# Performance work log

Measured on AMD Instinct MI355X. Metric: run time of the kernel, lower is better.

## Reference

```python
import jax, jax.numpy as jnp
import numpy as np

K = 3          # kernel_size
PAD = K // 2   # unfold padding
BN_EPS = 1e-5


def _conv(x, w, dilation, pad):
    # x: [B,C,H,W], w: [O,I,kh,kw]
    return jax.lax.conv_general_dilated(
        x, w, window_strides=(1, 1), padding=[(pad, pad), (pad, pad)],
        rhs_dilation=(dilation, dilation),
        dimension_numbers=("NCHW", "OIHW", "NCHW"))


def _bn(x, g, b, rm, rv):
    # eval-mode batchnorm with running stats
    inv = g / jnp.sqrt(rv + BN_EPS)
    return x * inv[None, :, None, None] + (b - rm * inv)[None, :, None, None]


def setup_inputs() -> dict:
    key = jax.random.key(0)
    ks = jax.random.split(key, 8)
    B, T, H, W = 8, 5, 512, 512
    mid = 16  # max(16, T // 4)
    inp = {
        "x_aligned": jax.random.normal(ks[0], (B, T, H, W), jnp.float32),
        "raw_diff": jax.random.normal(ks[1], (B, T - 1, H, W), jnp.float32),
        "w1": jax.random.normal(ks[2], (mid, T, 3, 3), jnp.float32) * 0.1,
        "g1": jnp.ones((mid,), jnp.float32), "b1": jnp.zeros((mid,), jnp.float32),
        "rm1": jnp.zeros((mid,), jnp.float32), "rv1": jnp.ones((mid,), jnp.float32),
        "w2": jax.random.normal(ks[3], (mid, mid, 3, 3), jnp.float32) * 0.1,
        "g2": jnp.ones((mid,), jnp.float32), "b2": jnp.zeros((mid,), jnp.float32),
        "rm2": jnp.zeros((mid,), jnp.float32), "rv2": jnp.ones((mid,), jnp.float32),
        "w3": jax.random.normal(ks[4], (mid, mid, 3, 3), jnp.float32) * 0.1,
        "g3": jnp.ones((mid,), jnp.float32), "b3": jnp.zeros((mid,), jnp.float32),
        "rm3": jnp.zeros((mid,), jnp.float32), "rv3": jnp.ones((mid,), jnp.float32),
        "w4": jax.random.normal(ks[5], (T * K * K, mid, 1, 1), jnp.float32) * 0.1,
        "bias": jnp.full((1,), -1.0, jnp.float32),
    }
    return inp


def reference(x_aligned, raw_diff, w1, g1, b1, rm1, rv1, w2, g2, b2, rm2, rv2,
              w3, g3, b3, rm3, rv3, w4, bias):
    B, T, H, W = x_aligned.shape
    # _accumulate: sequential abs-add == sum of abs over frame-diff axis
    acc = jnp.sum(jnp.abs(raw_diff), axis=1, keepdims=True)  # [B,1,H,W]
    mean = jnp.mean(acc)
    n = acc.size
    std = jnp.sqrt(jnp.sum((acc - mean) ** 2) / (n - 1))  # unbiased (torch default)
    motion = (acc - mean) / (std + 1e-6)
    motion_seq = jnp.broadcast_to(motion, (B, T, H, W))
    # _generate_kernel: conv+BN+ReLU stack with dilations 1,2,4 then 1x1
    h = jax.nn.relu(_bn(_conv(motion_seq, w1, 1, 1), g1, b1, rm1, rv1))
    h = jax.nn.relu(_bn(_conv(h, w2, 2, 2), g2, b2, rm2, rv2))
    h = jax.nn.relu(_bn(_conv(h, w3, 4, 4), g3, b3, rm3, rv3))
    raw_kernel = _conv(h, w4, 1, 0).reshape(B, T, K * K, H, W)
    kernel = (jax.nn.sigmoid(raw_kernel + bias[0]) + 0.01) * 10.0
    # _enhance: unfold (KxK patches, zero pad) then per-pixel weighted sum
    xp = jnp.pad(x_aligned, ((0, 0), (0, 0), (PAD, PAD), (PAD, PAD)))
    patches = jnp.stack(
        [xp[:, :, i:i + H, j:j + W] for i in range(K) for j in range(K)],
        axis=2)  # [B,T,K*K,H,W], matches F.unfold row-major kernel order
    return jnp.sum(kernel * patches, axis=2)  # [B,T,H,W]
```

## Files before the change

kernel.cpp:

```cpp
#include <hip/hip_runtime.h>
#include <hip/hip_bf16.h>
#include <math.h>

#define HH 512
#define WW 512
#define BB 8
#define TT 5
#define MID 16
#define HWSZ (HH*WW)
#define NPIX (BB*HWSZ)

typedef __attribute__((ext_vector_type(8))) short bf16x8;
typedef __attribute__((ext_vector_type(4))) float f32x4;

__device__ inline unsigned short f2bf(float f){
  unsigned u = __float_as_uint(f);
  u = u + 0x7fffu + ((u >> 16) & 1u);
  return (unsigned short)(u >> 16);
}
__device__ inline unsigned packpair(float a, float b){
  unsigned ua = __float_as_uint(a) + 0x8000u;
  unsigned ub = __float_as_uint(b) + 0x8000u;
  return __builtin_amdgcn_perm(ub, ua, 0x07060302u);
}
__device__ inline float blo(unsigned u){ return __uint_as_float(u << 16); }
__device__ inline float bhi(unsigned u){ return __uint_as_float(u & 0xffff0000u); }

union U4B { uint4 u; bf16x8 h; };


__global__ __launch_bounds__(256) void k_acc(const float* __restrict__ rd,
                                             float4* __restrict__ acc,
                                             float2* __restrict__ partial){
  int t = blockIdx.x * 256 + threadIdx.x;
  int i = t << 2;
  int b = i >> 18, p = i & (HWSZ - 1);
  const float* base = rd + (size_t)b * 4 * HWSZ + p;
  float4 f0 = *(const float4*)(base);
  float4 f1 = *(const float4*)(base + HWSZ);
  float4 f2 = *(const float4*)(base + 2*HWSZ);
  float4 f3 = *(const float4*)(base + 3*HWSZ);
  float4 s4;
  s4.x = fabsf(f0.x) + fabsf(f1.x) + fabsf(f2.x) + fabsf(f3.x);
  s4.y = fabsf(f0.y) + fabsf(f1.y) + fabsf(f2.y) + fabsf(f3.y);
  s4.z = fabsf(f0.z) + fabsf(f1.z) + fabsf(f2.z) + fabsf(f3.z);
  s4.w = fabsf(f0.w) + fabsf(f1.w) + fabsf(f2.w) + fabsf(f3.w);
  acc[t] = s4;
  float s  = s4.x + s4.y + s4.z + s4.w;
  float s2 = s4.x*s4.x + s4.y*s4.y + s4.z*s4.z + s4.w*s4.w;
  #pragma unroll
  for (int off = 32; off; off >>= 1){
    s  += __shfl_down(s,  off);
    s2 += __shfl_down(s2, off);
  }
  __shared__ float ls[4], ls2[4];
  int lane = threadIdx.x & 63, wid = threadIdx.x >> 6;
  if (lane == 0){ ls[wid] = s; ls2[wid] = s2; }
  __syncthreads();
  if (threadIdx.x == 0)
    partial[blockIdx.x] = make_float2(ls[0]+ls[1]+ls[2]+ls[3],
                                      ls2[0]+ls2[1]+ls2[2]+ls2[3]);
}

__global__ __launch_bounds__(256) void k_prep(const float2* __restrict__ partial,
    const float* __restrict__ w1, const float* __restrict__ w2, const float* __restrict__ w3,
    const float* __restrict__ g1, const float* __restrict__ b1, const float* __restrict__ rm1, const float* __restrict__ rv1,
    const float* __restrict__ g2, const float* __restrict__ b2, const float* __restrict__ rm2, const float* __restrict__ rv2,
    const float* __restrict__ g3, const float* __restrict__ b3, const float* __restrict__ rm3, const float* __restrict__ rv3,
    const float* __restrict__ w4, const float* __restrict__ bias0,
    float* __restrict__ cst, unsigned* __restrict__ wsB2, unsigned* __restrict__ wsB3,
    uint4* __restrict__ wsB4){
  int t = threadIdx.x;
  double s = 0.0, s2 = 0.0;
  for (int j = t; j < 2048; j += 256){
    float2 v = partial[j];
    s += (double)v.x; s2 += (double)v.y;
  }
  #pragma unroll
  for (int off = 32; off; off >>= 1){
    s  += __shfl_down(s,  off);
    s2 += __shfl_down(s2, off);
  }
  __shared__ double ds[4], ds2[4];
  int lane = t & 63, wid = t >> 6;
  if (lane == 0){ ds[wid] = s; ds2[wid] = s2; }
  __syncthreads();
  if (t == 0){
    double S  = ds[0]+ds[1]+ds[2]+ds[3];
    double S2 = ds2[0]+ds2[1]+ds2[2]+ds2[3];
    double n = (double)NPIX;
    double mean = S / n;
    double var  = (S2 - n * mean * mean) / (n - 1.0);
    double sd   = sqrt(var);
    cst[0] = (float)mean;
    cst[1] = (float)(1.0 / (sd + 1e-6));
    cst[242] = bias0[0];
  }
  if (t < 144){
    int c = t / 9, k = t % 9;
    float sw = 0.f;
    for (int f = 0; f < TT; f++) sw += w1[c*45 + f*9 + k];
    cst[2 + t] = sw;
  }
  if (t < 16){
    float s1 = g1[t] * rsqrtf(rv1[t] + 1e-5f);
    cst[146 + t] = s1; cst[162 + t] = b1[t] - rm1[t] * s1;
    float c2 = g2[t] * rsqrtf(rv2[t] + 1e-5f);
    cst[288 + t] = c2; cst[304 + t] = b2[t] - rm2[t] * c2;
    float c3 = g3[t] * rsqrtf(rv3[t] + 1e-5f);
    cst[320 + t] = c3; cst[336 + t] = b3[t] - rm3[t] * c3;
  }
  for (int it = 0; it < 5; it++){
    int idx = it * 256 + t;
    int m = idx >> 8, rem = idx & 255;
    int L = rem >> 2, jj = rem & 3;
    int out = L & 15, q = L >> 4;
    unsigned v2 = 0, v3 = 0;
    #pragma unroll
    for (int h = 0; h < 2; h++){
      int j = 2*jj + h;
      int k = q*8 + j;
      int tap = 2*m + (k >> 4);
      int ci = k & 15;
      unsigned bv2 = 0, bv3 = 0;
      if (tap < 9){
        bv2 = f2bf(w2[out*144 + ci*9 + tap]);
        bv3 = f2bf(w3[out*144 + ci*9 + tap]);
      }
      v2 |= bv2 << (16*h);
      v3 |= bv3 << (16*h);
    }
    wsB2[idx] = v2; wsB3[idx] = v3;
  }
  if (t < 192){
    int c = t >> 6, L = t & 63;
    int n = L & 15, q = L >> 4;
    int o = c*16 + n;
    unsigned vv[4];
    #pragma unroll
    for (int jj = 0; jj < 4; jj++){
      unsigned pk = 0;
      #pragma unroll
      for (int h = 0; h < 2; h++){
        int j = 2*jj + h, kci = q*8 + j;
        unsigned bv = 0;
        if (kci < 16 && o < 45) bv = f2bf(w4[o*16 + kci]);
        pk |= bv << (16*h);
      }
      vv[jj] = pk;
    }
    wsB4[c*64 + L] = make_uint4(vv[0], vv[1], vv[2], vv[3]);
  }
}

#define TR 12
#define TC 68
__global__ __launch_bounds__(256) void k_conv12(const float* __restrict__ acc,
                                                const float* __restrict__ C,
                                                const unsigned* __restrict__ wsB2,
                                                uint2* __restrict__ h2){
  __shared__ uint4 PL[2][TR*TC];
  int tid = threadIdx.x;
  int blk = blockIdx.x;
  int xt = blk & 7, yt = (blk >> 3) & 63, b = blk >> 9;
  int y0 = yt << 3, x0 = xt << 6;
  float mean = C[0], inv = C[1];
  const float* ab = acc + ((size_t)b << 18);
  #pragma unroll
  for (int it = 0; it < 4; it++){
    int i = it*256 + tid;
    if (i < TR*TC){
      int r = (i * 241) >> 14;
      int p = i - r*TC;
      int gy = y0 - 2 + r, gx = x0 - 2 + p;
      uint4 lo = make_uint4(0u,0u,0u,0u), hi = lo;
      if ((unsigned)gy < HH && (unsigned)gx < WW){
        float a[MID];
        #pragma unroll
        for (int o = 0; o < MID; o++) a[o] = 0.f;
        #pragma unroll
        for (int ky = 0; ky < 3; ky++){
          int yy = gy + ky - 1;
          if ((unsigned)yy >= HH) continue;
          #pragma unroll
          for (int kx = 0; kx < 3; kx++){
            int xx = gx + kx - 1;
            if ((unsigned)xx >= WW) continue;
            float m = (ab[(yy << 9) + xx] - mean) * inv;
            int k = ky * 3 + kx;
            #pragma unroll
            for (int o = 0; o < MID; o++) a[o] = fmaf(C[2 + o*9 + k], m, a[o]);
          }
        }
        unsigned pk[8];
        #pragma unroll
        for (int j = 0; j < 8; j++){
          float v0 = fmaxf(0.f, fmaf(a[2*j],   C[146 + 2*j],   C[162 + 2*j]));
          float v1 = fmaxf(0.f, fmaf(a[2*j+1], C[146 + 2*j+1], C[162 + 2*j+1]));
          pk[j] = packpair(v0, v1);
        }
        lo = make_uint4(pk[0], pk[1], pk[2], pk[3]);
        hi = make_uint4(pk[4], pk[5], pk[6], pk[7]);
      }
      PL[0][r*TC + p] = lo;
      PL[1][r*TC + p] = hi;
    }
  }
  __syncthreads();
  int lane = tid & 63, wv = tid >> 6;
  int col = lane & 15, q = lane >> 4;
  int chSel = q & 1;
  bool hiTap = (q >= 2);
  uint4 wfrag[5];
  #pragma unroll
  for (int m = 0; m < 5; m++) wfrag[m] = ((const uint4*)wsB2)[m*64 + lane];
  float4 sc = *(const float4*)&C[288 + q*4];
  float4 bi = *(const float4*)&C[304 + q*4];
  #pragma unroll
  for (int rr = 0; rr < 2; rr++){
    int ly = wv*2 + rr;
    #pragma unroll
    for (int g = 0; g < 4; g++){
      int lx = g << 4;
      f32x4 cc = {0.f, 0.f, 0.f, 0.f};
      #pragma unroll
      for (int m = 0; m < 5; m++){
        const int ta = 2*m, tb = 2*m + 1;
        int dy = (hiTap ? tb/3 : ta/3) - 1;
        int dx = (hiTap ? tb%3 : ta%3) - 1;
        bool tv = hiTap ? (tb < 9) : true;
        int trow = ly + 2 + 2*dy;
        int tpx  = lx + 2 + col + 2*dx;
        U4B bv; bv.u = PL[chSel][trow*TC + tpx];
        if (!tv) bv.u = make_uint4(0u,0u,0u,0u);
        U4B wb; wb.u = wfrag[m];
        cc = __builtin_amdgcn_mfma_f32_16x16x32_bf16(wb.h, bv.h, cc, 0, 0, 0);
      }
      float v0 = fmaxf(0.f, fmaf(cc[0], sc.x, bi.x));
      float v1 = fmaxf(0.f, fmaf(cc[1], sc.y, bi.y));
      float v2 = fmaxf(0.f, fmaf(cc[2], sc.z, bi.z));
      float v3 = fmaxf(0.f, fmaf(cc[3], sc.w, bi.w));
      int gy = y0 + ly, gx = x0 + lx + col;
      h2[(size_t)((b << 18) | (gy << 9) | gx)*4 + q] =
          make_uint2(packpair(v0, v1), packpair(v2, v3));
    }
  }
}

template<int DIL>
__device__ inline f32x4 convW(const uint4* __restrict__ hin, const uint4 wfrag[5],
                              int b, int y, int x0, int col, int q, f32x4 cc){
  int chSel = q & 1;
  bool hiTap = (q >= 2);
  #pragma unroll
  for (int m = 0; m < 5; m++){
    const int ta = 2*m, tb = 2*m + 1;
    int dy = (hiTap ? tb/3 : ta/3) - 1;
    int dx = (hiTap ? tb%3 : ta%3) - 1;
    bool tv = hiTap ? (tb < 9) : true;
    int yy = y + dy * DIL;
    int xx = x0 + col + dx * DIL;
    bool valid = tv && ((unsigned)yy < HH) && ((unsigned)xx < WW);
    U4B a; a.u = make_uint4(0u, 0u, 0u, 0u);
    if (valid) a.u = hin[(((unsigned)((b << 18) | (yy << 9) | xx)) << 1) | (unsigned)chSel];
    U4B bb; bb.u = wfrag[m];
    cc = __builtin_amdgcn_mfma_f32_16x16x32_bf16(bb.h, a.h, cc, 0, 0, 0);
  }
  return cc;
}

__global__ __launch_bounds__(256) void k_conv3m(const uint4* __restrict__ h2,
                                                const float* __restrict__ C,
                                                const unsigned* __restrict__ wsB3,
                                                const uint4* __restrict__ wsB4,
                                                const float* __restrict__ xal,
                                                float* __restrict__ out){
  __shared__ uint4 LB[4][640];
  int lane = threadIdx.x & 63, wv = threadIdx.x >> 6;
  char* myL = (char*)LB[wv];
  unsigned short* Lk = (unsigned short*)(myL + 3072);
  int w = blockIdx.x * 4 + wv;
  int base = w << 6;
  int b = base >> 18, rem = base & (HWSZ - 1);
  int y = rem >> 9, wx = rem & 511;
  uint4 wfrag[5];
  #pragma unroll
  for (int m = 0; m < 5; m++) wfrag[m] = ((const uint4*)wsB3)[m*64 + lane];
  uint4 bw[3];
  #pragma unroll
  for (int c = 0; c < 3; c++) bw[c] = wsB4[c*64 + lane];
  int col = lane & 15, q = lane >> 4;
  float4 sc = *(const float4*)&C[320 + q*4];
  float4 bi = *(const float4*)&C[336 + q*4];
  float cb = C[242];

  #pragma unroll
  for (int g = 0; g < 4; g++){
    f32x4 cc = {0.f, 0.f, 0.f, 0.f};
    cc = convW<4>(h2, wfrag, b, y, wx + g*16, col, q, cc);
    float v0 = fmaxf(0.f, fmaf(cc[0], sc.x, bi.x));
    float v1 = fmaxf(0.f, fmaf(cc[1], sc.y, bi.y));
    float v2 = fmaxf(0.f, fmaf(cc[2], sc.z, bi.z));
    float v3 = fmaxf(0.f, fmaf(cc[3], sc.w, bi.w));
    *(uint2*)(myL + (g*16 + col)*48 + q*8) = make_uint2(packpair(v0, v1), packpair(v2, v3));

    U4B a; a.u = make_uint4(0u, 0u, 0u, 0u);
    if (q < 2) a.u = *(const uint4*)(myL + (g*16 + col)*48 + q*16);
    #pragma unroll
    for (int c = 0; c < 3; c++){
      f32x4 aw = {cb, cb, cb, cb};
      U4B bb; bb.u = bw[c];
      aw = __builtin_amdgcn_mfma_f32_16x16x32_bf16(a.h, bb.h, aw, 0, 0, 0);
      #pragma unroll
      for (int r = 0; r < 4; r++){
        float e  = __expf(-aw[r]);
        float rc = __builtin_amdgcn_rcpf(1.f + e);
        float kern = fmaf(10.f, rc, 0.1f);
        unsigned u = __float_as_uint(kern) + 0x8000u;
        Lk[(g*16 + q*4 + r)*56 + c*16 + col] = (unsigned short)(u >> 16);
      }
    }
  }

  unsigned kvf[24];
  {
    const uint4* kp = (const uint4*)(myL + 3072 + lane*112);
    #pragma unroll
    for (int jj = 0; jj < 6; jj++){
      uint4 u = kp[jj];
      kvf[4*jj] = u.x; kvf[4*jj+1] = u.y; kvf[4*jj+2] = u.z; kvf[4*jj+3] = u.w;
    }
  }
  int px = wx + lane;
  bool mxl = (px > 0), mxr = (px < 511), mym = (y > 0), myp = (y < 511);
  bool msk[9] = { mym&&mxl, mym, mym&&mxr,
                  mxl,      true, mxr,
                  myp&&mxl, myp, myp&&mxr };
  int rowm = mym ? -2048 : 0;
  int rowp = myp ?  2048 : 0;
  int loff = mxl ? -4 : 0;
  int roff = mxr ?  4 : 0;
  const char* base0 = (const char*)(xal + ((size_t)(b*TT) << 18) + (y << 9) + px);
  #pragma unroll
  for (int t = 0; t < TT; t++){
    const char* pc = base0 + (size_t)t * (HWSZ*4);
    const char* pm = pc + rowm;
    const char* pp = pc + rowp;
    float xv[9];
    xv[0] = *(const float*)(pm + loff);
    xv[1] = *(const float*)(pm);
    xv[2] = *(const float*)(pm + roff);
    xv[3] = *(const float*)(pc + loff);
    xv[4] = *(const float*)(pc);
    xv[5] = *(const float*)(pc + roff);
    xv[6] = *(const float*)(pp + loff);
    xv[7] = *(const float*)(pp);
    xv[8] = *(const float*)(pp + roff);
    float ov = 0.f;
    #pragma unroll
    for (int k = 0; k < 9; k++){
      int n = t*9 + k;
      unsigned u = kvf[n >> 1];
      float kf = (n & 1) ? bhi(u) : blo(u);
      float kern = msk[k] ? kf : 0.f;
      ov = fmaf(kern, xv[k], ov);
    }
    out[((size_t)(b*TT + t) << 18) + (y << 9) + px] = ov;
  }
}

extern "C" void kernel_launch(void* const* d_in, const int* in_sizes, int n_in,
                              void* d_out, int out_size, void* d_ws, size_t ws_size,
                              hipStream_t stream){
  const float* xal = (const float*)d_in[0];
  const float* rd  = (const float*)d_in[1];
  const float* w1  = (const float*)d_in[2];
  const float* g1  = (const float*)d_in[3];
  const float* b1  = (const float*)d_in[4];
  const float* rm1 = (const float*)d_in[5];
  const float* rv1 = (const float*)d_in[6];
  const float* w2  = (const float*)d_in[7];
  const float* g2  = (const float*)d_in[8];
  const float* b2  = (const float*)d_in[9];
  const float* rm2 = (const float*)d_in[10];
  const float* rv2 = (const float*)d_in[11];
  const float* w3  = (const float*)d_in[12];
  const float* g3  = (const float*)d_in[13];
  const float* b3  = (const float*)d_in[14];
  const float* rm3 = (const float*)d_in[15];
  const float* rv3 = (const float*)d_in[16];
  const float* w4  = (const float*)d_in[17];
  const float* bias= (const float*)d_in[18];
  float* out = (float*)d_out;

  char* ws = (char*)d_ws;
  float2*   partial = (float2*)ws;
  float*    cst   = (float*)(ws + 16384);
  unsigned* wsB2  = (unsigned*)(ws + 32768);
  unsigned* wsB3  = (unsigned*)(ws + 40960);
  uint4*    wsB4  = (uint4*)(ws + 49152);
  float*    acc   = (float*)(ws + 65536);
  char*     h2    = (char*)(ws + 65536 + (size_t)NPIX*4);

  k_acc<<<2048, 256, 0, stream>>>(rd, (float4*)acc, partial);
  k_prep<<<1, 256, 0, stream>>>(partial, w1, w2, w3,
                                g1, b1, rm1, rv1,
                                g2, b2, rm2, rv2,
                                g3, b3, rm3, rv3, w4, bias, cst, wsB2, wsB3, wsB4);
  k_conv12<<<4096, 256, 0, stream>>>(acc, cst, wsB2, (uint2*)h2);
  k_conv3m<<<NPIX/256, 256, 0, stream>>>((const uint4*)h2, cst, wsB3, wsB4, xal, out);
}
```

Measured before the change: 272.4 us.

## Stage normalized motion tile in LDS for conv1 and shuffle conv3 output

In the fused conv1+conv2 kernel, the normalized motion values for a 14x72 halo tile are now loaded once into shared memory. The conv1 recompute then reads its 3x3 taps from LDS instead of issuing nine global loads per pixel with bounds checks. In the conv3 kernel, the bf16 activation transpose into MFMA A-operand layout now uses cross-lane shuffles instead of an LDS round trip, and the per-wave LDS buffer shrinks with a tighter kernel-weight stride. This cuts redundant global traffic and LDS usage, at the cost of an extra barrier, extra shared memory in conv12, and a possibly bank-conflicting 48-element stride.

```diff
diff --git a/kernel.cpp b/kernel.cpp
--- a/kernel.cpp
+++ b/kernel.cpp
@@ -159,6 +159,7 @@
                                                 const float* __restrict__ C,
                                                 const unsigned* __restrict__ wsB2,
                                                 uint2* __restrict__ h2){
+  __shared__ float AT[14*72];
   __shared__ uint4 PL[2][TR*TC];
   int tid = threadIdx.x;
   int blk = blockIdx.x;
@@ -168,11 +169,25 @@
   const float* ab = acc + ((size_t)b << 18);
   #pragma unroll
   for (int it = 0; it < 4; it++){
+    int idx = it*256 + tid;
+    if (idx < 14*72){
+      int r = (idx * 1821) >> 17;
+      int p = idx - r*72;
+      int gy = y0 - 3 + r, gx = x0 - 3 + p;
+      float v = 0.f;
+      if ((unsigned)gy < HH && (unsigned)gx < WW)
+        v = (ab[(gy << 9) + gx] - mean) * inv;
+      AT[idx] = v;
+    }
+  }
+  __syncthreads();
+  #pragma unroll
+  for (int it = 0; it < 4; it++){
     int i = it*256 + tid;
     if (i < TR*TC){
-      int r = (i * 241) >> 14;
-      int p = i - r*TC;
-      int gy = y0 - 2 + r, gx = x0 - 2 + p;
+      int r2 = (i * 241) >> 14;
+      int p2 = i - r2*TC;
+      int gy = y0 - 2 + r2, gx = x0 - 2 + p2;
       uint4 lo = make_uint4(0u,0u,0u,0u), hi = lo;
       if ((unsigned)gy < HH && (unsigned)gx < WW){
         float a[MID];
@@ -180,13 +195,9 @@
         for (int o = 0; o < MID; o++) a[o] = 0.f;
         #pragma unroll
         for (int ky = 0; ky < 3; ky++){
-          int yy = gy + ky - 1;
-          if ((unsigned)yy >= HH) continue;
           #pragma unroll
           for (int kx = 0; kx < 3; kx++){
-            int xx = gx + kx - 1;
-            if ((unsigned)xx >= WW) continue;
-            float m = (ab[(yy << 9) + xx] - mean) * inv;
+            float m = AT[(r2 + ky)*72 + (p2 + kx)];
             int k = ky * 3 + kx;
             #pragma unroll
             for (int o = 0; o < MID; o++) a[o] = fmaf(C[2 + o*9 + k], m, a[o]);
@@ -202,8 +213,8 @@
         lo = make_uint4(pk[0], pk[1], pk[2], pk[3]);
         hi = make_uint4(pk[4], pk[5], pk[6], pk[7]);
       }
-      PL[0][r*TC + p] = lo;
-      PL[1][r*TC + p] = hi;
+      PL[0][r2*TC + p2] = lo;
+      PL[1][r2*TC + p2] = hi;
     }
   }
   __syncthreads();
@@ -275,10 +286,10 @@
                                                 const uint4* __restrict__ wsB4,
                                                 const float* __restrict__ xal,
                                                 float* __restrict__ out){
-  __shared__ uint4 LB[4][640];
+  __shared__ uint4 LB[4][384];
   int lane = threadIdx.x & 63, wv = threadIdx.x >> 6;
   char* myL = (char*)LB[wv];
-  unsigned short* Lk = (unsigned short*)(myL + 3072);
+  unsigned short* Lk = (unsigned short*)myL;
   int w = blockIdx.x * 4 + wv;
   int base = w << 6;
   int b = base >> 18, rem = base & (HWSZ - 1);
@@ -293,6 +304,8 @@
   float4 sc = *(const float4*)&C[320 + q*4];
   float4 bi = *(const float4*)&C[336 + q*4];
   float cb = C[242];
+  int src0 = col + q*32;
+  int src1 = src0 + 16;
 
   #pragma unroll
   for (int g = 0; g < 4; g++){
@@ -302,10 +315,16 @@
     float v1 = fmaxf(0.f, fmaf(cc[1], sc.y, bi.y));
     float v2 = fmaxf(0.f, fmaf(cc[2], sc.z, bi.z));
     float v3 = fmaxf(0.f, fmaf(cc[3], sc.w, bi.w));
-    *(uint2*)(myL + (g*16 + col)*48 + q*8) = make_uint2(packpair(v0, v1), packpair(v2, v3));
-
-    U4B a; a.u = make_uint4(0u, 0u, 0u, 0u);
-    if (q < 2) a.u = *(const uint4*)(myL + (g*16 + col)*48 + q*16);
+    int pk01 = (int)packpair(v0, v1);
+    int pk23 = (int)packpair(v2, v3);
+
+    U4B a;
+    a.u.x = (unsigned)__shfl(pk01, src0);
+    a.u.y = (unsigned)__shfl(pk23, src0);
+    a.u.z = (unsigned)__shfl(pk01, src1);
+    a.u.w = (unsigned)__shfl(pk23, src1);
+    if (q >= 2) a.u = make_uint4(0u,0u,0u,0u);
+
     #pragma unroll
     for (int c = 0; c < 3; c++){
       f32x4 aw = {cb, cb, cb, cb};
@@ -317,14 +336,14 @@
         float rc = __builtin_amdgcn_rcpf(1.f + e);
         float kern = fmaf(10.f, rc, 0.1f);
         unsigned u = __float_as_uint(kern) + 0x8000u;
-        Lk[(g*16 + q*4 + r)*56 + c*16 + col] = (unsigned short)(u >> 16);
+        Lk[(g*16 + q*4 + r)*48 + c*16 + col] = (unsigned short)(u >> 16);
       }
     }
   }
 
   unsigned kvf[24];
   {
-    const uint4* kp = (const uint4*)(myL + 3072 + lane*112);
+    const uint4* kp = (const uint4*)(myL + lane*96);
     #pragma unroll
     for (int jj = 0; jj < 6; jj++){
       uint4 u = kp[jj];
```

New measurement: 260.8 us. 1.04x faster.
